# Performance work log

Hardware: AMD Instinct MI355X
Metric: run time of the kernel (lower is better)

The kernel has to match this reference:

```python
import jax, jax.numpy as jnp
import numpy as np

B, C_MEL, D_RES, TX, TY = 16, 80, 256, 1024, 4096
NEG = -1e9


def seq_mask(lengths, max_len):
    return (jnp.arange(max_len)[None, :] < lengths[:, None]).astype(jnp.float32)


def maximum_path(value, mask):
    # value, mask: [b, tx, ty]. Glow-TTS style monotonic-alignment Viterbi DP.
    b, t_x, t_y = value.shape
    value = value * mask
    x_range = jnp.arange(t_x)[None, :]  # [1, tx]

    def fwd_step(v, inp):
        val_j, j = inp  # val_j: [b, tx]
        v_prev = jnp.pad(v, ((0, 0), (1, 0)), constant_values=NEG)[:, :-1]  # v[x-1]
        stay = v >= v_prev  # True -> best path stays at same x
        v_max = jnp.where(stay, v, v_prev)
        v_new = jnp.where(x_range <= j, v_max + val_j, NEG)
        return v_new, stay

    _, stays = jax.lax.scan(
        fwd_step,
        jnp.zeros((b, t_x), value.dtype),
        (jnp.moveaxis(value, 2, 0), jnp.arange(t_y)),
    )  # stays: [ty, b, tx] bool
    mask_t = jnp.moveaxis(mask, 2, 0)  # [ty, b, tx]
    dirs = jnp.where(mask_t > 0, stays.astype(jnp.int32), 1)  # outside mask: stay

    idx0 = jnp.sum(mask[:, :, 0], axis=1).astype(jnp.int32) - 1  # x_length - 1
    barange = jnp.arange(b)

    def bwd_step(idx, dir_j):  # dir_j: [b, tx]
        row = jax.nn.one_hot(idx, t_x, dtype=value.dtype)  # [b, tx]
        idx_new = idx + dir_j[barange, idx] - 1
        return idx_new, row

    _, path = jax.lax.scan(bwd_step, idx0, dirs, reverse=True)  # [ty, b, tx]
    return jnp.transpose(path, (1, 2, 0)) * mask  # [b, tx, ty]


def setup_inputs() -> dict:
    key = jax.random.key(0)
    k1, k2, k3, k4, k5, k6 = jax.random.split(key, 6)
    return {
        "x_m": jax.random.normal(k1, (B, C_MEL, TX), jnp.float32),
        "x_res": jax.random.normal(k2, (B, D_RES, TX), jnp.float32),
        "mel": jax.random.normal(k3, (B, C_MEL, TY), jnp.float32),
        "x_lengths": jax.random.randint(k4, (B,), TX // 2, TX + 1, jnp.int32),
        "mel_lengths": jax.random.randint(k5, (B,), TY // 2, TY + 1, jnp.int32),
        "noise": jax.random.normal(k6, (B, C_MEL, TY), jnp.float32),
    }


def reference(x_m, x_res, mel, x_lengths, mel_lengths, noise):
    x_mask = seq_mask(x_lengths, TX)[:, None, :]   # [b, 1, tx]
    z_mask = seq_mask(mel_lengths, TY)[:, None, :]  # [b, 1, ty]
    attn_mask = x_mask[:, 0, :, None] * z_mask[:, 0, None, :]  # [b, tx, ty]

    # correlation-style score: -||x_m||^2 - ||mel||^2 + 2 x_m^T mel
    x2 = -jnp.sum(x_m ** 2, axis=1)[:, :, None]   # [b, tx, 1]
    z2 = -jnp.sum(mel ** 2, axis=1)[:, None, :]   # [b, 1, ty]
    xz2 = jnp.einsum("bct,bcs->bts", x_m, mel)    # [b, tx, ty]
    corr = x2 + z2 + 2.0 * xz2

    attn = maximum_path(corr, attn_mask)  # [b, tx, ty], no_grad in original

    z_m = jnp.einsum("bts,bct->bcs", attn, x_res)       # [b, d_res, ty]
    mel_proj = jnp.einsum("bts,bct->bcs", attn, x_m) + noise  # [b, n_mels, ty]
    mel_proj_loss = jnp.mean(jnp.abs((mel_proj - mel) * z_mask))
    logw_ = jnp.log(1e-8 + jnp.sum(attn, axis=-1))[:, None, :] * x_mask  # [b, 1, tx]
    return z_m, z_mask, attn, logw_, mel_proj_loss, mel_proj
```

## Files before the change

### kernel.cpp

```cpp
#include <hip/hip_runtime.h>
#include <cstdint>
#include <cstddef>

typedef unsigned int u32;
typedef unsigned short u16;

#define BB 16
#define CMEL 80
#define DRES 256
#define TXN 1024
#define TYN 4096
#define NEGV (-1e9f)

#define OFF_ZM    0ull
#define OFF_ZMASK 16777216ull
#define OFF_ATTN  16842752ull
#define OFF_LOGW  83951616ull
#define OFF_LOSS  83968000ull
#define OFF_MPROJ 83968001ull

#define WS_X2   0
#define WS_Z2   262144
#define WS_IDX  1310720
#define WS_PART 1572864

__global__ __launch_bounds__(1024) void k1_prep(
    const float* __restrict__ xm, const float* __restrict__ mel,
    const int* __restrict__ mlen,
    float* __restrict__ x2n, float* __restrict__ z2n, float* __restrict__ out_zmask) {
  int b = blockIdx.x;
  int slice = blockIdx.y;
  int t = threadIdx.x;
  if (slice == 0) {
    float acc = 0.f;
    const float* p = xm + (size_t)b * CMEL * TXN + t;
    #pragma unroll 4
    for (int c = 0; c < CMEL; ++c) { float v = p[(size_t)c * TXN]; acc = fmaf(v, v, acc); }
    x2n[b * TXN + t] = -acc;
  } else {
    int j = (slice - 1) * 1024 + t;
    float acc = 0.f;
    const float* p = mel + (size_t)b * CMEL * TYN + j;
    #pragma unroll 4
    for (int c = 0; c < CMEL; ++c) { float v = p[(size_t)c * TYN]; acc = fmaf(v, v, acc); }
    z2n[b * TYN + j] = -acc;
    out_zmask[b * TYN + j] = (j < mlen[b]) ? 1.0f : 0.0f;
  }
}

__global__ __launch_bounds__(256) void k2_corr(
    const float* __restrict__ xm, const float* __restrict__ mel,
    const float* __restrict__ x2n, const float* __restrict__ z2n,
    const int* __restrict__ xlen, const int* __restrict__ mlen,
    float* __restrict__ valT) {
  int b = blockIdx.z;
  int ml = mlen[b];
  int j0 = blockIdx.y * 128;
  if (j0 >= ml) return;
  int xl = xlen[b];
  int x0 = blockIdx.x * 128;

  __shared__ float sA[40][128];
  __shared__ float sB[40][128];

  int t = threadIdx.x;
  int i16 = t & 15, j16 = t >> 4;

  float acc[2][4][2][4];
  #pragma unroll
  for (int p = 0; p < 2; ++p)
    #pragma unroll
    for (int jj = 0; jj < 4; ++jj)
      #pragma unroll
      for (int q = 0; q < 2; ++q)
        #pragma unroll
        for (int i = 0; i < 4; ++i) acc[p][jj][q][i] = 0.f;

  for (int c0 = 0; c0 < CMEL; c0 += 40) {
    __syncthreads();
    for (int i = t; i < 40 * 32; i += 256) {
      int c = i >> 5, q = i & 31;
      *(float4*)&sA[c][q * 4] =
          *(const float4*)(xm + (size_t)(b * CMEL + c0 + c) * TXN + x0 + q * 4);
      *(float4*)&sB[c][q * 4] =
          *(const float4*)(mel + (size_t)(b * CMEL + c0 + c) * TYN + j0 + q * 4);
    }
    __syncthreads();
    #pragma unroll 2
    for (int c = 0; c < 40; ++c) {
      float av[2][4], bw[2][4];
      *(float4*)av[0] = *(const float4*)&sA[c][i16 * 4];
      *(float4*)av[1] = *(const float4*)&sA[c][64 + i16 * 4];
      *(float4*)bw[0] = *(const float4*)&sB[c][j16 * 4];
      *(float4*)bw[1] = *(const float4*)&sB[c][64 + j16 * 4];
      #pragma unroll
      for (int p = 0; p < 2; ++p)
        #pragma unroll
        for (int jj = 0; jj < 4; ++jj)
          #pragma unroll
          for (int q = 0; q < 2; ++q)
            #pragma unroll
            for (int i = 0; i < 4; ++i)
              acc[p][jj][q][i] = fmaf(av[q][i], bw[p][jj], acc[p][jj][q][i]);
    }
  }

  float4 xa[2];
  xa[0] = *(const float4*)(x2n + b * TXN + x0 + i16 * 4);
  xa[1] = *(const float4*)(x2n + b * TXN + x0 + 64 + i16 * 4);
  int xb0 = x0 + i16 * 4;
  int xb1 = x0 + 64 + i16 * 4;

  #pragma unroll
  for (int p = 0; p < 2; ++p)
    #pragma unroll
    for (int jj = 0; jj < 4; ++jj) {
      int j = j0 + p * 64 + j16 * 4 + jj;
      if (j >= ml) continue;
      float zz = z2n[b * TYN + j];
      float* row = valT + ((size_t)b * TYN + j) * TXN;
      float4 o;
      o.x = (xb0 + 0 < xl) ? ((xa[0].x + zz) + 2.f * acc[p][jj][0][0]) : 0.f;
      o.y = (xb0 + 1 < xl) ? ((xa[0].y + zz) + 2.f * acc[p][jj][0][1]) : 0.f;
      o.z = (xb0 + 2 < xl) ? ((xa[0].z + zz) + 2.f * acc[p][jj][0][2]) : 0.f;
      o.w = (xb0 + 3 < xl) ? ((xa[0].w + zz) + 2.f * acc[p][jj][0][3]) : 0.f;
      *(float4*)(row + xb0) = o;
      o.x = (xb1 + 0 < xl) ? ((xa[1].x + zz) + 2.f * acc[p][jj][1][0]) : 0.f;
      o.y = (xb1 + 1 < xl) ? ((xa[1].y + zz) + 2.f * acc[p][jj][1][1]) : 0.f;
      o.z = (xb1 + 2 < xl) ? ((xa[1].z + zz) + 2.f * acc[p][jj][1][2]) : 0.f;
      o.w = (xb1 + 3 < xl) ? ((xa[1].w + zz) + 2.f * acc[p][jj][1][3]) : 0.f;
      *(float4*)(row + xb1) = o;
    }
}

__global__ __launch_bounds__(512) void k3_dp(
    const float* __restrict__ valT, const int* __restrict__ mlen,
    u32* __restrict__ staysW) {
  int b = blockIdx.x;
  int ml = mlen[b];
  int t = threadIdx.x;
  int lane = t & 63, wid = t >> 6;
  int x0 = 2 * t, x1 = 2 * t + 1;
  __shared__ float edge[2][8];

  const float* base = valT + (size_t)b * TYN * TXN + x0;
  float v0 = 0.f, v1 = 0.f;
  float2 pf[16];
  #pragma unroll
  for (int k = 0; k < 16; ++k) pf[k] = *(const float2*)(base + (size_t)k * TXN);

  u32* sw0 = staysW + ((size_t)(b * TXN + x0) << 7);
  bool isLane0 = (lane == 0);
  bool isEdgeSrc = (lane == 63);
  int ewid = (wid > 0) ? (wid - 1) : 0;

  int jpad = (ml + 31) & ~31;
  for (int j0 = 0; j0 < jpad; j0 += 32) {
    u32 bits0 = 0, bits1 = 0;
    #pragma unroll
    for (int jj = 0; jj < 32; ++jj) {
      int j = j0 + jj;
      if (isEdgeSrc) edge[j & 1][wid] = v1;
      __syncthreads();
      float up = __shfl_up(v1, 1);
      float ev = edge[j & 1][ewid];
      float prev0 = isLane0 ? ((wid > 0) ? ev : NEGV) : up;
      float2 val = pf[jj & 15];
      int jl = j + 16;
      if (jl < ml) pf[jj & 15] = *(const float2*)(base + (size_t)jl * TXN);
      else          pf[jj & 15] = make_float2(0.f, 0.f);
      bool s0 = (v0 >= prev0);
      bool s1 = (v1 >= v0);
      float m0 = s0 ? v0 : prev0;
      float m1 = s1 ? v1 : v0;
      float nv0 = (x0 <= j) ? (m0 + val.x) : NEGV;
      float nv1 = (x1 <= j) ? (m1 + val.y) : NEGV;
      v0 = nv0; v1 = nv1;
      bits0 |= ((u32)s0) << jj;
      bits1 |= ((u32)s1) << jj;
    }
    sw0[j0 >> 5] = bits0;
    sw0[128 + (j0 >> 5)] = bits1;
  }
}

__global__ __launch_bounds__(256) void k4_backtrack(
    const u32* __restrict__ staysW, const int* __restrict__ xlen, const int* __restrict__ mlen,
    int* __restrict__ idxArr, float* __restrict__ out_logw) {
  int b = blockIdx.x;
  int xl = xlen[b], ml = mlen[b];
  int t = threadIdx.x;
  __shared__ u32 win[64][128];
  __shared__ u16 lidx[TYN];
  __shared__ u16 ldur[TXN];
  __shared__ int st[3];

  for (int i = t; i < TXN; i += 256) ldur[i] = 0;
  if (t == 0) { st[0] = xl - 1; st[1] = ml - 1; st[2] = ml - 1; }
  __syncthreads();

  int wb = (xl - 1) >> 6;
  for (int i = t; i < 64 * 128; i += 256) {
    int r = i >> 7, wq = i & 127;
    win[r][wq] = staysW[((size_t)(b * TXN + (wb << 6) + r) << 7) + wq];
  }
  __syncthreads();

  while (true) {
    if (t == 0) {
      int idx = st[0], j = st[1], end = st[2];
      while (j >= 0 && (idx >> 6) == wb) {
        u32 w = win[idx & 63][j >> 5];
        int p = j & 31;
        u32 below = w << (31 - p);
        u32 inv = ~below;
        int ones = (inv != 0u) ? __builtin_clz(inv) : 32;
        if (ones > p) {
          j -= p + 1;
        } else {
          int jz = j - ones;
          for (int q = jz; q <= end; ++q) lidx[q] = (u16)idx;
          ldur[idx] = (u16)(end - jz + 1);
          end = jz - 1;
          j = jz - 1;
          idx -= 1;
        }
      }
      if (j < 0) {
        for (int q = 0; q <= end; ++q) lidx[q] = (u16)idx;
        if (idx >= 0 && end >= 0) ldur[idx] = (u16)(end + 1);
        else if (idx >= 0) ldur[idx] = ldur[idx];
      }
      st[0] = idx; st[1] = j; st[2] = end;
    }
    __syncthreads();
    if (st[1] < 0) break;
    wb = st[0] >> 6;
    for (int i = t; i < 64 * 128; i += 256) {
      int r = i >> 7, wq = i & 127;
      win[r][wq] = staysW[((size_t)(b * TXN + (wb << 6) + r) << 7) + wq];
    }
    __syncthreads();
  }

  for (int q = t; q < TYN; q += 256) idxArr[b * TYN + q] = (q < ml) ? (int)lidx[q] : -1;
  for (int x = t; x < TXN; x += 256)
    out_logw[b * TXN + x] = (x < xl) ? logf(1e-8f + (float)ldur[x]) : 0.f;
}

__global__ __launch_bounds__(256) void k5_attn(
    const int* __restrict__ idxArr, float* __restrict__ attn) {
  int b = blockIdx.z;
  int x = blockIdx.y;
  int j = blockIdx.x * 1024 + threadIdx.x * 4;
  int4 iv = *(const int4*)(idxArr + b * TYN + j);
  float4 o;
  o.x = (iv.x == x) ? 1.f : 0.f;
  o.y = (iv.y == x) ? 1.f : 0.f;
  o.z = (iv.z == x) ? 1.f : 0.f;
  o.w = (iv.w == x) ? 1.f : 0.f;
  *(float4*)(attn + ((size_t)(b * TXN + x)) * TYN + j) = o;
}

__global__ __launch_bounds__(256) void k5_zm(
    const int* __restrict__ idxArr, const float* __restrict__ xres, float* __restrict__ zm) {
  int bid = blockIdx.x; int b = bid >> 8; int c = bid & 255;
  const float* row = xres + (size_t)(b * DRES + c) * TXN;
  float* orow = zm + (size_t)(b * DRES + c) * TYN;
  const int* ia = idxArr + b * TYN;
  for (int j = threadIdx.x; j < TYN; j += 256) {
    int idx = ia[j];
    orow[j] = (idx >= 0) ? row[idx] : 0.f;
  }
}

__global__ __launch_bounds__(256) void k5_mproj(
    const int* __restrict__ idxArr, const float* __restrict__ xm,
    const float* __restrict__ noise, const float* __restrict__ mel,
    float* __restrict__ mproj, float* __restrict__ partials) {
  int bid = blockIdx.x; int b = bid / CMEL; int c = bid % CMEL;
  const float* row  = xm    + (size_t)(b * CMEL + c) * TXN;
  const float* nrow = noise + (size_t)(b * CMEL + c) * TYN;
  const float* mrow = mel   + (size_t)(b * CMEL + c) * TYN;
  float* orow = mproj + (size_t)(b * CMEL + c) * TYN;
  const int* ia = idxArr + b * TYN;
  float acc = 0.f;
  for (int j = threadIdx.x; j < TYN; j += 256) {
    int idx = ia[j];
    float g = (idx >= 0) ? row[idx] : 0.f;
    float mp = g + nrow[j];
    orow[j] = mp;
    float d = mp - mrow[j];
    acc += (idx >= 0) ? fabsf(d) : 0.f;
  }
  #pragma unroll
  for (int o = 32; o; o >>= 1) acc += __shfl_down(acc, o);
  __shared__ float ws4[4];
  if ((threadIdx.x & 63) == 0) ws4[threadIdx.x >> 6] = acc;
  __syncthreads();
  if (threadIdx.x == 0) partials[bid] = (ws4[0] + ws4[1]) + (ws4[2] + ws4[3]);
}

__global__ __launch_bounds__(256) void k6_loss(
    const float* __restrict__ partials, float* __restrict__ out_loss) {
  float acc = 0.f;
  for (int i = threadIdx.x; i < BB * CMEL; i += 256) acc += partials[i];
  #pragma unroll
  for (int o = 32; o; o >>= 1) acc += __shfl_down(acc, o);
  __shared__ float ws4[4];
  if ((threadIdx.x & 63) == 0) ws4[threadIdx.x >> 6] = acc;
  __syncthreads();
  if (threadIdx.x == 0)
    out_loss[0] = ((ws4[0] + ws4[1]) + (ws4[2] + ws4[3])) * (1.0f / ((float)BB * CMEL * TYN));
}

extern "C" void kernel_launch(void* const* d_in, const int* in_sizes, int n_in,
                              void* d_out, int out_size, void* d_ws, size_t ws_size,
                              hipStream_t stream) {
  const float* xm    = (const float*)d_in[0];
  const float* xres  = (const float*)d_in[1];
  const float* mel   = (const float*)d_in[2];
  const int*   xlen  = (const int*)d_in[3];
  const int*   mlen  = (const int*)d_in[4];
  const float* noise = (const float*)d_in[5];

  float* out = (float*)d_out;
  float* out_zm    = out + OFF_ZM;
  float* out_zmask = out + OFF_ZMASK;
  float* out_attn  = out + OFF_ATTN;
  float* out_logw  = out + OFF_LOGW;
  float* out_loss  = out + OFF_LOSS;
  float* out_mproj = out + OFF_MPROJ;

  char* ws = (char*)d_ws;
  float* x2n      = (float*)(ws + WS_X2);
  float* z2n      = (float*)(ws + WS_Z2);
  int*   idxArr   = (int*)(ws + WS_IDX);
  float* partials = (float*)(ws + WS_PART);

  float* valT   = out_attn;
  u32*   staysW = (u32*)out_zm;

  hipLaunchKernelGGL(k1_prep, dim3(BB, 5), dim3(1024), 0, stream, xm, mel, mlen, x2n, z2n, out_zmask);
  hipLaunchKernelGGL(k2_corr, dim3(8, 32, BB), dim3(256), 0, stream, xm, mel, x2n, z2n, xlen, mlen, valT);
  hipLaunchKernelGGL(k3_dp, dim3(BB), dim3(512), 0, stream, valT, mlen, staysW);
  hipLaunchKernelGGL(k4_backtrack, dim3(BB), dim3(256), 0, stream, staysW, xlen, mlen, idxArr, out_logw);
  hipLaunchKernelGGL(k5_attn, dim3(4, TXN, BB), dim3(256), 0, stream, idxArr, out_attn);
  hipLaunchKernelGGL(k5_zm, dim3(BB * DRES), dim3(256), 0, stream, idxArr, xres, out_zm);
  hipLaunchKernelGGL(k5_mproj, dim3(BB * CMEL), dim3(256), 0, stream, idxArr, xm, noise, mel, out_mproj, partials);
  hipLaunchKernelGGL(k6_loss, dim3(1), dim3(256), 0, stream, partials, out_loss);
}
```

Baseline: 1.261 ms.

## Run Viterbi DP in one wavefront per batch to remove block barriers

The forward DP kernel now uses a single 64-lane wavefront per batch, with each lane owning 16 consecutive x positions held in registers. Only a wave shuffle passes the boundary value between lanes, so the per-step __syncthreads and shared-memory edge exchange are gone. The x<=j mask is replaced by resetting one newly activated slot per step, and loads are prefetched eight rows ahead as float4. In exchange, each step runs a serial 16-element chain per lane, register pressure rises, and each batch uses only one wave.

```diff
diff --git a/kernel.cpp b/kernel.cpp
--- a/kernel.cpp
+++ b/kernel.cpp
@@ -133,54 +133,82 @@
     }
 }
 
-__global__ __launch_bounds__(512) void k3_dp(
+__global__ __launch_bounds__(64) void k3_dp(
     const float* __restrict__ valT, const int* __restrict__ mlen,
     u32* __restrict__ staysW) {
   int b = blockIdx.x;
   int ml = mlen[b];
-  int t = threadIdx.x;
-  int lane = t & 63, wid = t >> 6;
-  int x0 = 2 * t, x1 = 2 * t + 1;
-  __shared__ float edge[2][8];
-
-  const float* base = valT + (size_t)b * TYN * TXN + x0;
-  float v0 = 0.f, v1 = 0.f;
-  float2 pf[16];
-  #pragma unroll
-  for (int k = 0; k < 16; ++k) pf[k] = *(const float2*)(base + (size_t)k * TXN);
-
-  u32* sw0 = staysW + ((size_t)(b * TXN + x0) << 7);
-  bool isLane0 = (lane == 0);
-  bool isEdgeSrc = (lane == 63);
-  int ewid = (wid > 0) ? (wid - 1) : 0;
-
+  int lane = threadIdx.x;
+  int xbase = lane << 4;
+
+  float v[16];
+  #pragma unroll
+  for (int i = 0; i < 16; ++i) v[i] = NEGV;
+  if (lane == 0) v[0] = 0.f;
+
+  float4 pf[8][4];
+  #pragma unroll
+  for (int k = 0; k < 8; ++k) {
+    const float* rowp = valT + (((size_t)(b * TYN + k)) << 10);
+    #pragma unroll
+    for (int q = 0; q < 4; ++q)
+      pf[k][q] = *(const float4*)(rowp + (xbase + (q << 2)));
+  }
+
+  u32* swb = staysW + (((size_t)(b * TXN + xbase)) << 7);
   int jpad = (ml + 31) & ~31;
+
   for (int j0 = 0; j0 < jpad; j0 += 32) {
-    u32 bits0 = 0, bits1 = 0;
+    u32 bits[16];
+    #pragma unroll
+    for (int i = 0; i < 16; ++i) bits[i] = 0;
+
     #pragma unroll
     for (int jj = 0; jj < 32; ++jj) {
-      int j = j0 + jj;
-      if (isEdgeSrc) edge[j & 1][wid] = v1;
-      __syncthreads();
-      float up = __shfl_up(v1, 1);
-      float ev = edge[j & 1][ewid];
-      float prev0 = isLane0 ? ((wid > 0) ? ev : NEGV) : up;
-      float2 val = pf[jj & 15];
-      int jl = j + 16;
-      if (jl < ml) pf[jj & 15] = *(const float2*)(base + (size_t)jl * TXN);
-      else          pf[jj & 15] = make_float2(0.f, 0.f);
-      bool s0 = (v0 >= prev0);
-      bool s1 = (v1 >= v0);
-      float m0 = s0 ? v0 : prev0;
-      float m1 = s1 ? v1 : v0;
-      float nv0 = (x0 <= j) ? (m0 + val.x) : NEGV;
-      float nv1 = (x1 <= j) ? (m1 + val.y) : NEGV;
-      v0 = nv0; v1 = nv1;
-      bits0 |= ((u32)s0) << jj;
-      bits1 |= ((u32)s1) << jj;
-    }
-    sw0[j0 >> 5] = bits0;
-    sw0[128 + (j0 >> 5)] = bits1;
+      const int j = j0 + jj;
+      float e = __shfl_up(v[15], 1);
+      if (lane == 0) e = NEGV;
+
+      float val[16];
+      #pragma unroll
+      for (int q = 0; q < 4; ++q) {
+        val[4 * q + 0] = pf[jj & 7][q].x;
+        val[4 * q + 1] = pf[jj & 7][q].y;
+        val[4 * q + 2] = pf[jj & 7][q].z;
+        val[4 * q + 3] = pf[jj & 7][q].w;
+      }
+
+      #pragma unroll
+      for (int i = 15; i >= 1; --i) {
+        bool s = v[i] >= v[i - 1];
+        float m = s ? v[i] : v[i - 1];
+        v[i] = m + val[i];
+        bits[i] |= ((u32)s) << jj;
+      }
+      {
+        bool s = v[0] >= e;
+        float m = s ? v[0] : e;
+        v[0] = m + val[0];
+        bits[0] |= ((u32)s) << jj;
+      }
+
+      {
+        int lt = (j + 1) >> 4;
+        if (lane == lt) v[(jj + 1) & 15] = NEGV;
+      }
+
+      {
+        int jn = j + 8; if (jn > TYN - 1) jn = TYN - 1;
+        const float* rowp = valT + (((size_t)(b * TYN + jn)) << 10);
+        #pragma unroll
+        for (int q = 0; q < 4; ++q)
+          pf[jj & 7][q] = *(const float4*)(rowp + (xbase + (q << 2)));
+      }
+    }
+
+    const int w = j0 >> 5;
+    #pragma unroll
+    for (int i = 0; i < 16; ++i) swb[(i << 7) + w] = bits[i];
   }
 }
 
@@ -229,7 +257,6 @@
       if (j < 0) {
         for (int q = 0; q <= end; ++q) lidx[q] = (u16)idx;
         if (idx >= 0 && end >= 0) ldur[idx] = (u16)(end + 1);
-        else if (idx >= 0) ldur[idx] = ldur[idx];
       }
       st[0] = idx; st[1] = j; st[2] = end;
     }
@@ -343,7 +370,7 @@
 
   hipLaunchKernelGGL(k1_prep, dim3(BB, 5), dim3(1024), 0, stream, xm, mel, mlen, x2n, z2n, out_zmask);
   hipLaunchKernelGGL(k2_corr, dim3(8, 32, BB), dim3(256), 0, stream, xm, mel, x2n, z2n, xlen, mlen, valT);
-  hipLaunchKernelGGL(k3_dp, dim3(BB), dim3(512), 0, stream, valT, mlen, staysW);
+  hipLaunchKernelGGL(k3_dp, dim3(BB), dim3(64), 0, stream, valT, mlen, staysW);
   hipLaunchKernelGGL(k4_backtrack, dim3(BB), dim3(256), 0, stream, staysW, xlen, mlen, idxArr, out_logw);
   hipLaunchKernelGGL(k5_attn, dim3(4, TXN, BB), dim3(256), 0, stream, idxArr, out_attn);
   hipLaunchKernelGGL(k5_zm, dim3(BB * DRES), dim3(256), 0, stream, idxArr, xres, out_zm);
```

After: 1.202 ms. 1.05x faster.
